# Optimization experiments

Measured on AMD Instinct MI355X. Metric: run time of the kernel, lower is better.

The kernel has to match this reference:

```python
import jax, jax.numpy as jnp
import numpy as np

N = 100000      # nodes
E = 1600000     # directed edges (avg degree 16)
D_IN = 128
D_H = 128


def setup_inputs() -> dict:
    key = jax.random.key(0)
    k1, k2, k3 = jax.random.split(key, 3)
    x = jax.random.normal(k1, (N, D_IN), dtype=jnp.float32)
    edge_index = jax.random.randint(k2, (2, E), 0, N, dtype=jnp.int32)
    # GCNConv linear (glorot-ish) and bias (zeros, as in PyG init)
    W = jax.random.normal(k3, (D_IN, D_H), dtype=jnp.float32) / np.float32(np.sqrt(D_IN))
    b = jnp.zeros((D_H,), dtype=jnp.float32)
    return {"x": x, "edge_index": edge_index, "W": W, "b": b}


def reference(x, edge_index, W, b):
    # GCNConv: h = D^{-1/2} (A + I) D^{-1/2} X W + b ; then ReLU
    h = x @ W                                  # [N, D_H] transform first (PyG order)
    loop = jnp.arange(N, dtype=edge_index.dtype)
    src = jnp.concatenate([edge_index[0], loop])   # message sources (x_j)
    dst = jnp.concatenate([edge_index[1], loop])   # aggregation targets
    ones = jnp.ones(src.shape[0], dtype=h.dtype)
    deg = jax.ops.segment_sum(ones, dst, num_segments=N)          # in-degree incl. self-loop
    dis = jnp.where(deg > 0, jax.lax.rsqrt(deg), 0.0)             # deg^{-1/2}
    norm = dis[src] * dis[dst]                                    # [E+N]
    msgs = h[src] * norm[:, None]                                 # edge-level gather (memory bound)
    out = jax.ops.segment_sum(msgs, dst, num_segments=N) + b      # scatter-add aggregate
    return jax.nn.relu(out)
```

## Files before the change

### kernel.cpp

```cpp
#include <hip/hip_runtime.h>

#define NN 100000
#define NE 1600000
#define NB 196
#define BSH 9
#define CAPB 12288
#define CAPC 14336

typedef unsigned int u32;
typedef unsigned short u16;
typedef short short8 __attribute__((ext_vector_type(8)));
typedef float floatx4 __attribute__((ext_vector_type(4)));

__device__ __forceinline__ float bf2f(u16 h) { return __uint_as_float((u32)h << 16); }
__device__ __forceinline__ u16 f2bf(float f) {
    u32 u = __float_as_uint(f);
    return (u16)((u + 0x7fffu + ((u >> 16) & 1u)) >> 16);
}
__device__ __forceinline__ float2 bf2(u32 v) {
    return make_float2(__uint_as_float(v << 16), __uint_as_float(v & 0xffff0000u));
}

__global__ __launch_bounds__(256) void k_zero(int* gcur) {
    int i = threadIdx.x;
    if (i < NB) gcur[i] = 0;
}

__global__ __launch_bounds__(256) void k_prepW(const float* __restrict__ W, u16* __restrict__ wtb) {
    int t = blockIdx.x * 256 + threadIdx.x;
    if (t >= 128 * 128) return;
    int n = t >> 7, k = t & 127;
    float v = W[k * 128 + n];
    u32 byteoff = (u32)n * 256 + (((u32)k * 2) ^ (u32)((n & 7) << 4));
    wtb[byteoff >> 1] = f2bf(v);
}

__global__ __launch_bounds__(1024) void k_binA(const int* __restrict__ src, const int* __restrict__ dst,
                                               int* __restrict__ gcur, u32* __restrict__ staging) {
    __shared__ int hist[NB];
    __shared__ int cur[NB];
    int t = threadIdx.x;
    int base = blockIdx.x * 8192;
    for (int i = t; i < NB; i += 1024) hist[i] = 0;
    __syncthreads();
    u32 pk[8];
    int bk[8];
#pragma unroll
    for (int j = 0; j < 8; ++j) {
        int e = base + j * 1024 + t;
        bk[j] = -1;
        if (e < NE) {
            int s = src[e], d = dst[e];
            bk[j] = d >> BSH;
            pk[j] = ((u32)(d & 511) << 17) | (u32)s;
            atomicAdd(&hist[bk[j]], 1);
        }
    }
    __syncthreads();
    for (int i = t; i < NB; i += 1024) {
        int h = hist[i];
        cur[i] = h ? atomicAdd(&gcur[i], h) : 0;
    }
    __syncthreads();
#pragma unroll
    for (int j = 0; j < 8; ++j) {
        if (bk[j] >= 0) {
            int pos = atomicAdd(&cur[bk[j]], 1);
            if (pos < CAPB) staging[(size_t)bk[j] * CAPB + pos] = pk[j];
        }
    }
}

__global__ __launch_bounds__(256) void k_passB(const u32* __restrict__ staging, const int* __restrict__ gcur,
                                               int* __restrict__ col, int* __restrict__ startA,
                                               int* __restrict__ ecnt, float* __restrict__ dis) {
    __shared__ int cnt[512];
    __shared__ int loc[512];
    __shared__ int total;
    int b = blockIdx.x, t = threadIdx.x;
    int bcnt = gcur[b];
    if (bcnt > CAPB) bcnt = CAPB;
    for (int i = t; i < 512; i += 256) cnt[i] = 0;
    if (t == 0) total = 0;
    __syncthreads();
    const u32* st = staging + (size_t)b * CAPB;
    for (int i = t; i < bcnt; i += 256) atomicAdd(&cnt[st[i] >> 17], 1);
    __syncthreads();
    for (int i = t; i < 512; i += 256) {
        int c = cnt[i];
        loc[i] = atomicAdd(&total, (c + 3) & ~3);
    }
    __syncthreads();
    int cbase = b * CAPC;
    for (int i = t; i < 512; i += 256) {
        int node = (b << BSH) + i;
        if (node < NN) {
            startA[node] = cbase + loc[i];
            ecnt[node]   = cnt[i];
            dis[node]    = rsqrtf((float)cnt[i] + 1.0f);
        }
    }
    __syncthreads();
    for (int i = t; i < 512; i += 256) cnt[i] = loc[i];
    __syncthreads();
    for (int i = t; i < bcnt; i += 256) {
        u32 p = st[i];
        int pos = atomicAdd(&cnt[p >> 17], 1);
        col[cbase + pos] = (int)(p & 0x1ffffu);
    }
}

__global__ __launch_bounds__(256) void k_gemm(const float* __restrict__ x, const u16* __restrict__ wtb,
                                              const float* __restrict__ dis, u16* __restrict__ g) {
    __shared__ char smem[65536];
    char* xh = smem;
    char* xl = smem + 16384;
    char* wt = smem + 32768;
    int t = threadIdx.x;
    int r0 = blockIdx.x * 64;

    {
        const float4* s4 = (const float4*)wtb;
        float4* d4 = (float4*)wt;
#pragma unroll
        for (int i = 0; i < 8; ++i) d4[t + i * 256] = s4[t + i * 256];
    }
    {
        const float4* x4 = (const float4*)x;
        int c4 = t & 31, rb = t >> 5;
#pragma unroll
        for (int p = 0; p < 8; ++p) {
            int r = rb + p * 8;
            int gr = r0 + r;
            float4 v = (gr < NN) ? x4[(size_t)gr * 32 + c4] : make_float4(0.f, 0.f, 0.f, 0.f);
            u16 h0 = f2bf(v.x), h1 = f2bf(v.y), h2 = f2bf(v.z), h3 = f2bf(v.w);
            u16 q0 = f2bf(v.x - bf2f(h0)), q1 = f2bf(v.y - bf2f(h1));
            u16 q2 = f2bf(v.z - bf2f(h2)), q3 = f2bf(v.w - bf2f(h3));
            u32 off = (u32)r * 256 + (((u32)c4 * 8) ^ (u32)((r & 7) << 4));
            *(uint2*)(xh + off) = make_uint2((u32)h0 | ((u32)h1 << 16), (u32)h2 | ((u32)h3 << 16));
            *(uint2*)(xl + off) = make_uint2((u32)q0 | ((u32)q1 << 16), (u32)q2 | ((u32)q3 << 16));
        }
    }
    __syncthreads();

    int w = t >> 6, l = t & 63;
    int lr = l & 15;
    int hi2 = l >> 4;
    int arow = w * 16 + lr;
    u32 aswz = (u32)((arow & 7) << 4);
    floatx4 acc[8];
#pragma unroll
    for (int nt = 0; nt < 8; ++nt) acc[nt] = (floatx4){0.f, 0.f, 0.f, 0.f};

#pragma unroll
    for (int kc = 0; kc < 4; ++kc) {
        u32 akoff = (u32)(kc * 64 + hi2 * 16);
        short8 ah = *(short8*)(xh + (u32)arow * 256 + (akoff ^ aswz));
        short8 al = *(short8*)(xl + (u32)arow * 256 + (akoff ^ aswz));
#pragma unroll
        for (int nt = 0; nt < 8; ++nt) {
            int brow = nt * 16 + lr;
            short8 bv = *(short8*)(wt + (u32)brow * 256 + (akoff ^ (u32)((brow & 7) << 4)));
            acc[nt] = __builtin_amdgcn_mfma_f32_16x16x32_bf16(ah, bv, acc[nt], 0, 0, 0);
            acc[nt] = __builtin_amdgcn_mfma_f32_16x16x32_bf16(al, bv, acc[nt], 0, 0, 0);
        }
    }

    int rbase = r0 + w * 16 + hi2 * 4;
#pragma unroll
    for (int q = 0; q < 4; ++q) {
        int grow = rbase + q;
        if (grow < NN) {
            float d = dis[grow];
#pragma unroll
            for (int nt = 0; nt < 8; ++nt) {
                g[(size_t)grow * 128 + nt * 16 + lr] = f2bf(d * acc[nt][q]);
            }
        }
    }
}

__global__ __launch_bounds__(256) void k_aggr(const u32* __restrict__ g, const int* __restrict__ col,
                                              const int* __restrict__ start, const int* __restrict__ ecnt,
                                              const float* __restrict__ dis, const float* __restrict__ b,
                                              float* __restrict__ out) {
    int wv = (blockIdx.x * 256 + threadIdx.x) >> 6;
    int l = threadIdx.x & 63;
    int node = wv * 2 + (l >> 5);
    int sl = l & 31;
    if (node >= NN) return;
    const uint2* g2 = (const uint2*)g;
    int s = start[node], cnt = ecnt[node];

    uint2 sv = g2[(size_t)node * 32 + sl];
    float2 p0 = bf2(sv.x), p1 = bf2(sv.y);
    float4 acc = make_float4(p0.x, p0.y, p1.x, p1.y);

    int e = 0;
    for (; e + 4 <= cnt; e += 4) {
        int4 ss = *(const int4*)&col[s + e];
        uint2 a0 = g2[(size_t)ss.x * 32 + sl];
        uint2 a1 = g2[(size_t)ss.y * 32 + sl];
        uint2 a2 = g2[(size_t)ss.z * 32 + sl];
        uint2 a3 = g2[(size_t)ss.w * 32 + sl];
        float2 u0 = bf2(a0.x), v0 = bf2(a0.y), u1 = bf2(a1.x), v1 = bf2(a1.y);
        float2 u2 = bf2(a2.x), v2 = bf2(a2.y), u3 = bf2(a3.x), v3 = bf2(a3.y);
        acc.x += (u0.x + u1.x) + (u2.x + u3.x);
        acc.y += (u0.y + u1.y) + (u2.y + u3.y);
        acc.z += (v0.x + v1.x) + (v2.x + v3.x);
        acc.w += (v0.y + v1.y) + (v2.y + v3.y);
    }
    for (; e < cnt; ++e) {
        int sc = col[s + e];
        uint2 a = g2[(size_t)sc * 32 + sl];
        float2 u = bf2(a.x), v = bf2(a.y);
        acc.x += u.x; acc.y += u.y; acc.z += v.x; acc.w += v.y;
    }

    float di = dis[node];
    float4 bb = *(const float4*)&b[sl * 4];
    float4 o;
    o.x = fmaxf(fmaf(di, acc.x, bb.x), 0.f);
    o.y = fmaxf(fmaf(di, acc.y, bb.y), 0.f);
    o.z = fmaxf(fmaf(di, acc.z, bb.z), 0.f);
    o.w = fmaxf(fmaf(di, acc.w, bb.w), 0.f);
    *(float4*)&out[(size_t)node * 128 + sl * 4] = o;
}

extern "C" void kernel_launch(void* const* d_in, const int* in_sizes, int n_in,
                              void* d_out, int out_size, void* d_ws, size_t ws_size,
                              hipStream_t stream) {
    const float* x = (const float*)d_in[0];
    const int* ei = (const int*)d_in[1];
    const float* W = (const float*)d_in[2];
    const float* b = (const float*)d_in[3];
    float* out = (float*)d_out;
    const int* srcA = ei;
    const int* dstA = ei + NE;

    char* ws = (char*)d_ws;
    size_t off = 0;
    auto take = [&](size_t bytes) -> char* {
        char* p = ws + off;
        off = (off + bytes + 255) & ~(size_t)255;
        return p;
    };
    u16*   g      = (u16*)  take((size_t)NN * 128 * 2);
    float* dis    = (float*)take((size_t)NN * 4);
    int*   ecnt   = (int*)  take((size_t)NN * 4);
    int*   startA = (int*)  take((size_t)NN * 4);
    int*   colA   = (int*)  take((size_t)NB * CAPC * 4);
    int*   gcur   = (int*)  take(256 * 4);
    u16*   wtb    = (u16*)  take(128 * 128 * 2);

    u32* staging = (u32*)g;

    k_prepW<<<64, 256, 0, stream>>>(W, wtb);
    k_zero <<<1, 256, 0, stream>>>(gcur);
    k_binA <<<(NE + 8191) / 8192, 1024, 0, stream>>>(srcA, dstA, gcur, staging);
    k_passB<<<NB, 256, 0, stream>>>(staging, gcur, colA, startA, ecnt, dis);
    k_gemm <<<(NN + 63) / 64, 256, 0, stream>>>(x, wtb, dis, g);
    k_aggr <<<(NN / 2 + 3) / 4, 256, 0, stream>>>((const u32*)g, colA, startA, ecnt, dis, b, out);
}
```

Measured before the change: 144.8 us.

## Widen aggregation gathers to 16B per lane, unroll by eight, fuse zero kernel

The aggregation kernel now assigns 16 lanes per node, each loading 16 bytes (8 bf16 values), so one wave handles 4 nodes instead of 2. The edge loop is unrolled by 8 with two accumulator sets, keeping more gathers in flight and shortening dependency chains. Column-index loads use nontemporal hints and the output stores are nontemporal. The separate zeroing kernel is folded into k_prepW to save one launch. In exchange, each lane holds more live registers, which may lower occupancy.

```diff
diff --git a/kernel.cpp b/kernel.cpp
--- a/kernel.cpp
+++ b/kernel.cpp
@@ -11,6 +11,8 @@
 typedef unsigned short u16;
 typedef short short8 __attribute__((ext_vector_type(8)));
 typedef float floatx4 __attribute__((ext_vector_type(4)));
+typedef int intx4 __attribute__((ext_vector_type(4)));
+typedef float fltx4 __attribute__((ext_vector_type(4)));
 
 __device__ __forceinline__ float bf2f(u16 h) { return __uint_as_float((u32)h << 16); }
 __device__ __forceinline__ u16 f2bf(float f) {
@@ -20,14 +22,16 @@
 __device__ __forceinline__ float2 bf2(u32 v) {
     return make_float2(__uint_as_float(v << 16), __uint_as_float(v & 0xffff0000u));
 }
-
-__global__ __launch_bounds__(256) void k_zero(int* gcur) {
-    int i = threadIdx.x;
-    if (i < NB) gcur[i] = 0;
-}
-
-__global__ __launch_bounds__(256) void k_prepW(const float* __restrict__ W, u16* __restrict__ wtb) {
+__device__ __forceinline__ void acc8(float4& A, float4& B, uint4 a) {
+    float2 u0 = bf2(a.x), u1 = bf2(a.y), u2 = bf2(a.z), u3 = bf2(a.w);
+    A.x += u0.x; A.y += u0.y; A.z += u1.x; A.w += u1.y;
+    B.x += u2.x; B.y += u2.y; B.z += u3.x; B.w += u3.y;
+}
+
+__global__ __launch_bounds__(256) void k_prepW(const float* __restrict__ W, u16* __restrict__ wtb,
+                                               int* __restrict__ gcur) {
     int t = blockIdx.x * 256 + threadIdx.x;
+    if (t < NB) gcur[t] = 0;
     if (t >= 128 * 128) return;
     int n = t >> 7, k = t & 127;
     float v = W[k * 128 + n];
@@ -186,45 +190,76 @@
                                               float* __restrict__ out) {
     int wv = (blockIdx.x * 256 + threadIdx.x) >> 6;
     int l = threadIdx.x & 63;
-    int node = wv * 2 + (l >> 5);
-    int sl = l & 31;
+    int node = wv * 4 + (l >> 4);
+    int sl = l & 15;
     if (node >= NN) return;
-    const uint2* g2 = (const uint2*)g;
+    const uint4* g4 = (const uint4*)g;
     int s = start[node], cnt = ecnt[node];
 
-    uint2 sv = g2[(size_t)node * 32 + sl];
-    float2 p0 = bf2(sv.x), p1 = bf2(sv.y);
-    float4 acc = make_float4(p0.x, p0.y, p1.x, p1.y);
+    uint4 sv = g4[(size_t)node * 16 + sl];
+    float2 t0 = bf2(sv.x), t1 = bf2(sv.y), t2 = bf2(sv.z), t3 = bf2(sv.w);
+    float4 accA = make_float4(t0.x, t0.y, t1.x, t1.y);
+    float4 accB = make_float4(t2.x, t2.y, t3.x, t3.y);
 
     int e = 0;
-    for (; e + 4 <= cnt; e += 4) {
-        int4 ss = *(const int4*)&col[s + e];
-        uint2 a0 = g2[(size_t)ss.x * 32 + sl];
-        uint2 a1 = g2[(size_t)ss.y * 32 + sl];
-        uint2 a2 = g2[(size_t)ss.z * 32 + sl];
-        uint2 a3 = g2[(size_t)ss.w * 32 + sl];
-        float2 u0 = bf2(a0.x), v0 = bf2(a0.y), u1 = bf2(a1.x), v1 = bf2(a1.y);
-        float2 u2 = bf2(a2.x), v2 = bf2(a2.y), u3 = bf2(a3.x), v3 = bf2(a3.y);
-        acc.x += (u0.x + u1.x) + (u2.x + u3.x);
-        acc.y += (u0.y + u1.y) + (u2.y + u3.y);
-        acc.z += (v0.x + v1.x) + (v2.x + v3.x);
-        acc.w += (v0.y + v1.y) + (v2.y + v3.y);
+    if (cnt >= 8) {
+        float4 ac2A = make_float4(0.f, 0.f, 0.f, 0.f);
+        float4 ac2B = make_float4(0.f, 0.f, 0.f, 0.f);
+        for (; e + 8 <= cnt; e += 8) {
+            intx4 c0 = __builtin_nontemporal_load((const intx4*)&col[s + e]);
+            intx4 c1 = __builtin_nontemporal_load((const intx4*)&col[s + e + 4]);
+            uint4 a0 = g4[(size_t)c0.x * 16 + sl];
+            uint4 a1 = g4[(size_t)c0.y * 16 + sl];
+            uint4 a2 = g4[(size_t)c0.z * 16 + sl];
+            uint4 a3 = g4[(size_t)c0.w * 16 + sl];
+            uint4 a4 = g4[(size_t)c1.x * 16 + sl];
+            uint4 a5 = g4[(size_t)c1.y * 16 + sl];
+            uint4 a6 = g4[(size_t)c1.z * 16 + sl];
+            uint4 a7 = g4[(size_t)c1.w * 16 + sl];
+            acc8(accA, accB, a0);
+            acc8(ac2A, ac2B, a1);
+            acc8(accA, accB, a2);
+            acc8(ac2A, ac2B, a3);
+            acc8(accA, accB, a4);
+            acc8(ac2A, ac2B, a5);
+            acc8(accA, accB, a6);
+            acc8(ac2A, ac2B, a7);
+        }
+        accA.x += ac2A.x; accA.y += ac2A.y; accA.z += ac2A.z; accA.w += ac2A.w;
+        accB.x += ac2B.x; accB.y += ac2B.y; accB.z += ac2B.z; accB.w += ac2B.w;
+    }
+    if (e + 4 <= cnt) {
+        intx4 c0 = __builtin_nontemporal_load((const intx4*)&col[s + e]);
+        uint4 a0 = g4[(size_t)c0.x * 16 + sl];
+        uint4 a1 = g4[(size_t)c0.y * 16 + sl];
+        uint4 a2 = g4[(size_t)c0.z * 16 + sl];
+        uint4 a3 = g4[(size_t)c0.w * 16 + sl];
+        acc8(accA, accB, a0);
+        acc8(accA, accB, a1);
+        acc8(accA, accB, a2);
+        acc8(accA, accB, a3);
+        e += 4;
     }
     for (; e < cnt; ++e) {
         int sc = col[s + e];
-        uint2 a = g2[(size_t)sc * 32 + sl];
-        float2 u = bf2(a.x), v = bf2(a.y);
-        acc.x += u.x; acc.y += u.y; acc.z += v.x; acc.w += v.y;
+        uint4 a = g4[(size_t)sc * 16 + sl];
+        acc8(accA, accB, a);
     }
 
     float di = dis[node];
-    float4 bb = *(const float4*)&b[sl * 4];
-    float4 o;
-    o.x = fmaxf(fmaf(di, acc.x, bb.x), 0.f);
-    o.y = fmaxf(fmaf(di, acc.y, bb.y), 0.f);
-    o.z = fmaxf(fmaf(di, acc.z, bb.z), 0.f);
-    o.w = fmaxf(fmaf(di, acc.w, bb.w), 0.f);
-    *(float4*)&out[(size_t)node * 128 + sl * 4] = o;
+    float4 b0 = *(const float4*)&b[sl * 8];
+    float4 b1 = *(const float4*)&b[sl * 8 + 4];
+    fltx4 o0, o1;
+    o0.x = fmaxf(fmaf(di, accA.x, b0.x), 0.f);
+    o0.y = fmaxf(fmaf(di, accA.y, b0.y), 0.f);
+    o0.z = fmaxf(fmaf(di, accA.z, b0.z), 0.f);
+    o0.w = fmaxf(fmaf(di, accA.w, b0.w), 0.f);
+    o1.x = fmaxf(fmaf(di, accB.x, b1.x), 0.f);
+    o1.y = fmaxf(fmaf(di, accB.y, b1.y), 0.f);
+    o1.z = fmaxf(fmaf(di, accB.z, b1.z), 0.f);
+    o1.w = fmaxf(fmaf(di, accB.w, b1.w), 0.f);
+    __builtin_nontemporal_store(o0, (fltx4*)&out[(size_t)node * 128 + sl * 8]);
+    __builtin_nontemporal_store(o1, (fltx4*)&out[(size_t)node * 128 + sl * 8 + 4]);
 }
 
 extern "C" void kernel_launch(void* const* d_in, const int* in_sizes, int n_in,
@@ -255,10 +290,9 @@
 
     u32* staging = (u32*)g;
 
-    k_prepW<<<64, 256, 0, stream>>>(W, wtb);
-    k_zero <<<1, 256, 0, stream>>>(gcur);
+    k_prepW<<<64, 256, 0, stream>>>(W, wtb, gcur);
     k_binA <<<(NE + 8191) / 8192, 1024, 0, stream>>>(srcA, dstA, gcur, staging);
     k_passB<<<NB, 256, 0, stream>>>(staging, gcur, colA, startA, ecnt, dis);
     k_gemm <<<(NN + 63) / 64, 256, 0, stream>>>(x, wtb, dis, g);
-    k_aggr <<<(NN / 2 + 3) / 4, 256, 0, stream>>>((const u32*)g, colA, startA, ecnt, dis, b, out);
-}
+    k_aggr <<<(NN + 15) / 16, 256, 0, stream>>>((const u32*)g, colA, startA, ecnt, dis, b, out);
+}
```

Result: no change. 144.1 us (-0.5%).

## Slice feature matrix into 16-column panels for cache-local gather aggregation

Applied to the files above, without the earlier changes.

The GEMM output g is stored as 8 column slices of 16 features per node (slice-major), and aggregation launches 8 blocks per node chunk, with each block handling one slice using 4 lanes per node. Each slice is 3.2 MB, so the random gathers are meant to stay within L2/MALL for their slice instead of touching the full 25.6 MB matrix. The edge loop is unrolled to 8 with two accumulators, the output store is nontemporal, and the zero kernel is folded into prepW to drop one launch. The cost is that each node's column indices are read 8 times, and each gather fetches only 8 bytes per lane.

```diff
diff --git a/kernel.cpp b/kernel.cpp
--- a/kernel.cpp
+++ b/kernel.cpp
@@ -11,6 +11,8 @@
 typedef unsigned short u16;
 typedef short short8 __attribute__((ext_vector_type(8)));
 typedef float floatx4 __attribute__((ext_vector_type(4)));
+typedef int intx4 __attribute__((ext_vector_type(4)));
+typedef float fltx4 __attribute__((ext_vector_type(4)));
 
 __device__ __forceinline__ float bf2f(u16 h) { return __uint_as_float((u32)h << 16); }
 __device__ __forceinline__ u16 f2bf(float f) {
@@ -20,14 +22,15 @@
 __device__ __forceinline__ float2 bf2(u32 v) {
     return make_float2(__uint_as_float(v << 16), __uint_as_float(v & 0xffff0000u));
 }
-
-__global__ __launch_bounds__(256) void k_zero(int* gcur) {
-    int i = threadIdx.x;
-    if (i < NB) gcur[i] = 0;
-}
-
-__global__ __launch_bounds__(256) void k_prepW(const float* __restrict__ W, u16* __restrict__ wtb) {
+__device__ __forceinline__ void acc4(float4& A, uint2 a) {
+    float2 u0 = bf2(a.x), u1 = bf2(a.y);
+    A.x += u0.x; A.y += u0.y; A.z += u1.x; A.w += u1.y;
+}
+
+__global__ __launch_bounds__(256) void k_prepW(const float* __restrict__ W, u16* __restrict__ wtb,
+                                               int* __restrict__ gcur) {
     int t = blockIdx.x * 256 + threadIdx.x;
+    if (t < NB) gcur[t] = 0;
     if (t >= 128 * 128) return;
     int n = t >> 7, k = t & 127;
     float v = W[k * 128 + n];
@@ -174,7 +177,7 @@
             float d = dis[grow];
 #pragma unroll
             for (int nt = 0; nt < 8; ++nt) {
-                g[(size_t)grow * 128 + nt * 16 + lr] = f2bf(d * acc[nt][q]);
+                g[((size_t)nt * NN + (size_t)grow) * 16 + lr] = f2bf(d * acc[nt][q]);
             }
         }
     }
@@ -184,47 +187,66 @@
                                               const int* __restrict__ start, const int* __restrict__ ecnt,
                                               const float* __restrict__ dis, const float* __restrict__ b,
                                               float* __restrict__ out) {
-    int wv = (blockIdx.x * 256 + threadIdx.x) >> 6;
-    int l = threadIdx.x & 63;
-    int node = wv * 2 + (l >> 5);
-    int sl = l & 31;
+    int slice = blockIdx.x & 7;
+    int chunk = blockIdx.x >> 3;
+    int t = threadIdx.x;
+    int l = t & 63;
+    int node = chunk * 64 + (t >> 6) * 16 + (l >> 2);
+    int q = l & 3;
     if (node >= NN) return;
-    const uint2* g2 = (const uint2*)g;
+    const uint2* gs = (const uint2*)g + (size_t)slice * NN * 4;
     int s = start[node], cnt = ecnt[node];
 
-    uint2 sv = g2[(size_t)node * 32 + sl];
-    float2 p0 = bf2(sv.x), p1 = bf2(sv.y);
-    float4 acc = make_float4(p0.x, p0.y, p1.x, p1.y);
+    float4 acc;
+    {
+        uint2 sv = gs[(size_t)node * 4 + q];
+        float2 u0 = bf2(sv.x), u1 = bf2(sv.y);
+        acc = make_float4(u0.x, u0.y, u1.x, u1.y);
+    }
 
     int e = 0;
-    for (; e + 4 <= cnt; e += 4) {
-        int4 ss = *(const int4*)&col[s + e];
-        uint2 a0 = g2[(size_t)ss.x * 32 + sl];
-        uint2 a1 = g2[(size_t)ss.y * 32 + sl];
-        uint2 a2 = g2[(size_t)ss.z * 32 + sl];
-        uint2 a3 = g2[(size_t)ss.w * 32 + sl];
-        float2 u0 = bf2(a0.x), v0 = bf2(a0.y), u1 = bf2(a1.x), v1 = bf2(a1.y);
-        float2 u2 = bf2(a2.x), v2 = bf2(a2.y), u3 = bf2(a3.x), v3 = bf2(a3.y);
-        acc.x += (u0.x + u1.x) + (u2.x + u3.x);
-        acc.y += (u0.y + u1.y) + (u2.y + u3.y);
-        acc.z += (v0.x + v1.x) + (v2.x + v3.x);
-        acc.w += (v0.y + v1.y) + (v2.y + v3.y);
+    if (cnt >= 8) {
+        float4 ac2 = make_float4(0.f, 0.f, 0.f, 0.f);
+        for (; e + 8 <= cnt; e += 8) {
+            intx4 c0 = *(const intx4*)&col[s + e];
+            intx4 c1 = *(const intx4*)&col[s + e + 4];
+            uint2 a0 = gs[(size_t)c0.x * 4 + q];
+            uint2 a1 = gs[(size_t)c0.y * 4 + q];
+            uint2 a2 = gs[(size_t)c0.z * 4 + q];
+            uint2 a3 = gs[(size_t)c0.w * 4 + q];
+            uint2 a4 = gs[(size_t)c1.x * 4 + q];
+            uint2 a5 = gs[(size_t)c1.y * 4 + q];
+            uint2 a6 = gs[(size_t)c1.z * 4 + q];
+            uint2 a7 = gs[(size_t)c1.w * 4 + q];
+            acc4(acc, a0); acc4(ac2, a1);
+            acc4(acc, a2); acc4(ac2, a3);
+            acc4(acc, a4); acc4(ac2, a5);
+            acc4(acc, a6); acc4(ac2, a7);
+        }
+        acc.x += ac2.x; acc.y += ac2.y; acc.z += ac2.z; acc.w += ac2.w;
+    }
+    if (e + 4 <= cnt) {
+        intx4 c0 = *(const intx4*)&col[s + e];
+        uint2 a0 = gs[(size_t)c0.x * 4 + q];
+        uint2 a1 = gs[(size_t)c0.y * 4 + q];
+        uint2 a2 = gs[(size_t)c0.z * 4 + q];
+        uint2 a3 = gs[(size_t)c0.w * 4 + q];
+        acc4(acc, a0); acc4(acc, a1); acc4(acc, a2); acc4(acc, a3);
+        e += 4;
     }
     for (; e < cnt; ++e) {
-        int sc = col[s + e];
-        uint2 a = g2[(size_t)sc * 32 + sl];
-        float2 u = bf2(a.x), v = bf2(a.y);
-        acc.x += u.x; acc.y += u.y; acc.z += v.x; acc.w += v.y;
+        uint2 a = gs[(size_t)col[s + e] * 4 + q];
+        acc4(acc, a);
     }
 
     float di = dis[node];
-    float4 bb = *(const float4*)&b[sl * 4];
-    float4 o;
+    float4 bb = *(const float4*)&b[slice * 16 + q * 4];
+    fltx4 o;
     o.x = fmaxf(fmaf(di, acc.x, bb.x), 0.f);
     o.y = fmaxf(fmaf(di, acc.y, bb.y), 0.f);
     o.z = fmaxf(fmaf(di, acc.z, bb.z), 0.f);
     o.w = fmaxf(fmaf(di, acc.w, bb.w), 0.f);
-    *(float4*)&out[(size_t)node * 128 + sl * 4] = o;
+    __builtin_nontemporal_store(o, (fltx4*)&out[(size_t)node * 128 + slice * 16 + q * 4]);
 }
 
 extern "C" void kernel_launch(void* const* d_in, const int* in_sizes, int n_in,
@@ -255,10 +277,9 @@
 
     u32* staging = (u32*)g;
 
-    k_prepW<<<64, 256, 0, stream>>>(W, wtb);
-    k_zero <<<1, 256, 0, stream>>>(gcur);
+    k_prepW<<<64, 256, 0, stream>>>(W, wtb, gcur);
     k_binA <<<(NE + 8191) / 8192, 1024, 0, stream>>>(srcA, dstA, gcur, staging);
     k_passB<<<NB, 256, 0, stream>>>(staging, gcur, colA, startA, ecnt, dis);
     k_gemm <<<(NN + 63) / 64, 256, 0, stream>>>(x, wtb, dis, g);
-    k_aggr <<<(NN / 2 + 3) / 4, 256, 0, stream>>>((const u32*)g, colA, startA, ecnt, dis, b, out);
-}
+    k_aggr <<<8 * ((NN + 63) / 64), 256, 0, stream>>>((const u32*)g, colA, startA, ecnt, dis, b, out);
+}
```

Result: slower. 162.0 us (+11.9%).
